# Kernel tuning notes

Measured on AMD Instinct MI355X. Metric: run time of the kernel, lower is better.

## Reference

```python
import jax, jax.numpy as jnp
import numpy as np
import math

B, NPG, DEG = 100, 500, 12          # graphs, nodes/graph, avg degree
F_IN, H, C = 128, 128, 10
RATIO = 0.5
N = B * NPG
E = N * DEG
K1 = math.ceil(NPG * RATIO)          # 250
K2 = math.ceil(K1 * RATIO)           # 125
K3 = math.ceil(K2 * RATIO)           # 63


def _lin(k, i, o):
    return jax.random.uniform(k, (i, o), jnp.float32, -1.0, 1.0) / np.sqrt(i).astype(np.float32)


def setup_inputs() -> dict:
    key = jax.random.key(0)
    ks = jax.random.split(key, 16)
    x = jax.random.normal(ks[0], (N, F_IN), jnp.float32)
    off = (jnp.arange(B, dtype=jnp.int32) * NPG)[:, None]
    src = (jax.random.randint(ks[1], (B, NPG * DEG), 0, NPG, jnp.int32) + off).reshape(-1)
    dst = (jax.random.randint(ks[2], (B, NPG * DEG), 0, NPG, jnp.int32) + off).reshape(-1)
    edge_index = jnp.stack([src, dst])
    return {
        'x': x, 'edge_index': edge_index,
        'Wl1': _lin(ks[3], F_IN, H), 'bl1': jnp.zeros((H,), jnp.float32), 'Wr1': _lin(ks[4], F_IN, H),
        'Wl2': _lin(ks[5], H, H), 'bl2': jnp.zeros((H,), jnp.float32), 'Wr2': _lin(ks[6], H, H),
        'Wl3': _lin(ks[7], H, H), 'bl3': jnp.zeros((H,), jnp.float32), 'Wr3': _lin(ks[8], H, H),
        'pw1': jax.random.normal(ks[9], (H,), jnp.float32),
        'pw2': jax.random.normal(ks[10], (H,), jnp.float32),
        'pw3': jax.random.normal(ks[11], (H,), jnp.float32),
        'W1': _lin(ks[12], 2 * H, H), 'b1': jnp.zeros((H,), jnp.float32),
        'W2': _lin(ks[13], H, H // 2), 'b2': jnp.zeros((H // 2,), jnp.float32),
        'W3': _lin(ks[14], H // 2, C), 'b3': jnp.zeros((C,), jnp.float32),
    }


def sage_conv(x, src, dst, emask, Wl, bl, Wr, n_nodes):
    # PyG SAGEConv: out_i = lin_l(mean_{j->i} x_j) + lin_r(x_i)
    msg = x[src] * emask[:, None]                                   # [E, d]
    agg = jax.ops.segment_sum(msg, dst, num_segments=n_nodes)
    cnt = jax.ops.segment_sum(emask, dst, num_segments=n_nodes)
    mean = agg / jnp.maximum(cnt, 1.0)[:, None]
    return mean @ Wl + bl + x @ Wr


def topk_pool(x, w, src, dst, emask, n_per, k):
    # TopKPooling: score = tanh(x.w/||w||); keep top-k nodes per graph; x_kept *= score
    score = jnp.tanh((x @ w) / jnp.linalg.norm(w))                  # [B*n_per]
    topv, topi = jax.lax.top_k(score.reshape(B, n_per), k)          # [B, k]
    perm = (topi + (jnp.arange(B, dtype=jnp.int32) * n_per)[:, None]).reshape(-1)
    x_new = x[perm] * topv.reshape(-1)[:, None]                     # [B*k, d]
    mapping = jnp.full((B * n_per,), -1, jnp.int32).at[perm].set(jnp.arange(B * k, dtype=jnp.int32))
    ns, nd = mapping[src], mapping[dst]
    emask_new = emask * ((ns >= 0) & (nd >= 0)).astype(emask.dtype)
    return x_new, jnp.maximum(ns, 0), jnp.maximum(nd, 0), emask_new


def readout(x, k):
    # global_max_pool || global_mean_pool (all graphs have exactly k nodes)
    xr = x.reshape(B, k, H)
    return jnp.concatenate([xr.max(axis=1), xr.mean(axis=1)], axis=1)  # [B, 2H]


def reference(x, edge_index, Wl1, bl1, Wr1, Wl2, bl2, Wr2, Wl3, bl3, Wr3,
              pw1, pw2, pw3, W1, b1, W2, b2, W3, b3):
    src, dst = edge_index[0], edge_index[1]
    emask = jnp.ones((E,), jnp.float32)
    h = jax.nn.relu(sage_conv(x, src, dst, emask, Wl1, bl1, Wr1, N))
    h, src, dst, emask = topk_pool(h, pw1, src, dst, emask, NPG, K1)
    x1 = readout(h, K1)
    h = jax.nn.relu(sage_conv(h, src, dst, emask, Wl2, bl2, Wr2, B * K1))
    h, src, dst, emask = topk_pool(h, pw2, src, dst, emask, K1, K2)
    x2 = readout(h, K2)
    h = jax.nn.relu(sage_conv(h, src, dst, emask, Wl3, bl3, Wr3, B * K2))
    h, src, dst, emask = topk_pool(h, pw3, src, dst, emask, K2, K3)
    x3 = readout(h, K3)
    z = x1 + x2 + x3
    z = jax.nn.relu(z @ W1 + b1)   # dropout is identity in eval mode
    z = jax.nn.relu(z @ W2 + b2)
    return jax.nn.log_softmax(z @ W3 + b3, axis=1)   # pool_loss == 0 for TopKPool
```

## Files before the change

### kernel.cpp

```cpp
#include <hip/hip_runtime.h>
#include <math.h>

#define BG    100
#define NPG   500
#define FD    128
#define EE    600000
#define EPG   6000
#define NN    50000
#define K1    250
#define K2    125
#define K3    63
#define CAP   64

typedef short v8s __attribute__((ext_vector_type(8)));
typedef float v4f __attribute__((ext_vector_type(4)));

__device__ __forceinline__ int swz(int p, int N) {
    int j = p & 7, i = p >> 3;
    int chunk = N >> 3, rem = N & 7;
    int mj = j < rem ? j : rem;
    return j * chunk + mj + i;
}

__device__ __forceinline__ unsigned short f2bf(float f) {
    unsigned int u = __float_as_uint(f);
    unsigned int r = (u + 0x7FFFu + ((u >> 16) & 1u)) >> 16;
    return (unsigned short)r;
}
__device__ __forceinline__ float bf2f(unsigned short b) {
    return __uint_as_float(((unsigned int)b) << 16);
}

__global__ void prep_w_kernel(const float* __restrict__ Wl1, const float* __restrict__ Wr1,
                              const float* __restrict__ Wl2, const float* __restrict__ Wr2,
                              const float* __restrict__ Wl3, const float* __restrict__ Wr3,
                              unsigned short* __restrict__ wt_hi, unsigned short* __restrict__ wt_lo) {
    int id = blockIdx.x * blockDim.x + threadIdx.x;
    if (id >= 3 * 256 * 128) return;
    int layer = id >> 15, rem = id & 32767;
    int k = rem >> 7, n = rem & 127;
    const float* Wl = layer == 0 ? Wl1 : (layer == 1 ? Wl2 : Wl3);
    const float* Wr = layer == 0 ? Wr1 : (layer == 1 ? Wr2 : Wr3);
    float w = (k < 128) ? Wl[k * 128 + n] : Wr[(k - 128) * 128 + n];
    unsigned short hi = f2bf(w);
    unsigned short lo = f2bf(w - bf2f(hi));
    long long o = (long long)layer * 32768 + n * 256 + k;
    wt_hi[o] = hi;
    wt_lo[o] = lo;
}

__global__ __launch_bounds__(1024) void fill_first_kernel(const int* __restrict__ ei,
                                                          int* __restrict__ deg,
                                                          int* __restrict__ col) {
    __shared__ int lcnt[NPG];
    int b = swz(blockIdx.x, BG), tid = threadIdx.x;
    for (int i = tid; i < NPG; i += 1024) lcnt[i] = 0;
    __syncthreads();
    for (int e0 = tid; e0 < EPG; e0 += 1024) {
        int e = b * EPG + e0;
        int d = ei[EE + e];
        int pos = atomicAdd(&lcnt[d - b * NPG], 1);
        if (pos < CAP) col[(long long)d * CAP + pos] = ei[e];
    }
    __syncthreads();
    for (int i = tid; i < NPG; i += 1024) deg[b * NPG + i] = lcnt[i];
}

__global__ void gather_agg_kernel(const int* __restrict__ deg, const int* __restrict__ col,
                                  const float* __restrict__ x, float* __restrict__ mean,
                                  int n, int NB) {
    int g = swz(blockIdx.x, NB) * 256 + threadIdx.x;
    int node = g >> 5, sub = g & 31;
    if (node >= n) return;
    int d = deg[node]; if (d > CAP) d = CAP;
    const int* cp = col + (long long)node * CAP;
    float ax = 0.0f, ay = 0.0f, az = 0.0f, aw = 0.0f;
    int j = 0;
    for (; j + 4 <= d; j += 4) {
        int s0 = cp[j], s1 = cp[j + 1], s2 = cp[j + 2], s3 = cp[j + 3];
        float4 v0 = ((const float4*)(x + (long long)s0 * FD))[sub];
        float4 v1 = ((const float4*)(x + (long long)s1 * FD))[sub];
        float4 v2 = ((const float4*)(x + (long long)s2 * FD))[sub];
        float4 v3 = ((const float4*)(x + (long long)s3 * FD))[sub];
        ax += v0.x; ay += v0.y; az += v0.z; aw += v0.w;
        ax += v1.x; ay += v1.y; az += v1.z; aw += v1.w;
        ax += v2.x; ay += v2.y; az += v2.z; aw += v2.w;
        ax += v3.x; ay += v3.y; az += v3.z; aw += v3.w;
    }
    for (; j < d; ++j) {
        float4 v = ((const float4*)(x + (long long)cp[j] * FD))[sub];
        ax += v.x; ay += v.y; az += v.z; aw += v.w;
    }
    float inv = 1.0f / fmaxf((float)d, 1.0f);
    float4 o; o.x = ax * inv; o.y = ay * inv; o.z = az * inv; o.w = aw * inv;
    ((float4*)(mean + (long long)node * FD))[sub] = o;
}

__global__ __launch_bounds__(256) void sage_gemm_mfma_kernel(
        const float* __restrict__ mean, const float* __restrict__ x,
        const unsigned short* __restrict__ wt_hi, const unsigned short* __restrict__ wt_lo,
        const float* __restrict__ bl, const float* __restrict__ pw,
        float* __restrict__ hout, float* __restrict__ score, int M, int NB) {
    __shared__ unsigned short Ah[64 * 40], Al[64 * 40];
    __shared__ unsigned short Bh[128 * 40], Bl[128 * 40];
    __shared__ float spart[64 * 16];
    __shared__ float snrmp[16];
    int tid  = threadIdx.x;
    int wave = tid >> 6, lane = tid & 63;
    int quad = lane >> 4, l15 = lane & 15;
    int row0 = swz(blockIdx.x, NB) * 64;

    v4f acc[8];
#pragma unroll
    for (int t = 0; t < 8; t++) acc[t] = (v4f){0.f, 0.f, 0.f, 0.f};

    if (tid < 16) {
        float s = 0.f;
#pragma unroll
        for (int t = 0; t < 8; t++) { float p = pw[t * 16 + tid]; s += p * p; }
        snrmp[tid] = s;
    }

    int arow = tid >> 2;
    int ak   = (tid & 3) * 8;
    int growA = row0 + arow; if (growA > M - 1) growA = M - 1;
    int brow = tid >> 1;
    int bk   = (tid & 1) * 16;

    for (int kt = 0; kt < 8; ++kt) {
        {
            const float* Ab = (kt < 4) ? mean : x;
            const float* ap = Ab + (long long)growA * FD + ((kt < 4) ? kt : kt - 4) * 32 + ak;
            float4 v0 = *(const float4*)(ap);
            float4 v1 = *(const float4*)(ap + 4);
            float f[8] = {v0.x, v0.y, v0.z, v0.w, v1.x, v1.y, v1.z, v1.w};
            ushort4 h0, h1, l0, l1;
            unsigned short hb[8], lb[8];
#pragma unroll
            for (int q = 0; q < 8; q++) {
                hb[q] = f2bf(f[q]);
                lb[q] = f2bf(f[q] - bf2f(hb[q]));
            }
            h0 = make_ushort4(hb[0], hb[1], hb[2], hb[3]);
            h1 = make_ushort4(hb[4], hb[5], hb[6], hb[7]);
            l0 = make_ushort4(lb[0], lb[1], lb[2], lb[3]);
            l1 = make_ushort4(lb[4], lb[5], lb[6], lb[7]);
            *(ushort4*)&Ah[arow * 40 + ak]     = h0;
            *(ushort4*)&Ah[arow * 40 + ak + 4] = h1;
            *(ushort4*)&Al[arow * 40 + ak]     = l0;
            *(ushort4*)&Al[arow * 40 + ak + 4] = l1;
        }
        {
            int klog = kt * 32;
            const uint4* sh = (const uint4*)(wt_hi + (long long)brow * 256 + klog + bk);
            const uint4* sl = (const uint4*)(wt_lo + (long long)brow * 256 + klog + bk);
            uint4 vh0 = sh[0], vh1 = sh[1];
            uint4 vl0 = sl[0], vl1 = sl[1];
            *(uint4*)&Bh[brow * 40 + bk]     = vh0;
            *(uint4*)&Bh[brow * 40 + bk + 8] = vh1;
            *(uint4*)&Bl[brow * 40 + bk]     = vl0;
            *(uint4*)&Bl[brow * 40 + bk + 8] = vl1;
        }
        __syncthreads();
        v8s a_h = *(const v8s*)&Ah[(16 * wave + l15) * 40 + quad * 8];
        v8s a_l = *(const v8s*)&Al[(16 * wave + l15) * 40 + quad * 8];
#pragma unroll
        for (int t = 0; t < 8; t++) {
            v8s b_h = *(const v8s*)&Bh[(t * 16 + l15) * 40 + quad * 8];
            v8s b_l = *(const v8s*)&Bl[(t * 16 + l15) * 40 + quad * 8];
            acc[t] = __builtin_amdgcn_mfma_f32_16x16x32_bf16(a_l, b_h, acc[t], 0, 0, 0);
            acc[t] = __builtin_amdgcn_mfma_f32_16x16x32_bf16(a_h, b_l, acc[t], 0, 0, 0);
            acc[t] = __builtin_amdgcn_mfma_f32_16x16x32_bf16(a_h, b_h, acc[t], 0, 0, 0);
        }
        __syncthreads();
    }

    int rbase = row0 + 16 * wave + quad * 4;
    float part[4] = {0.f, 0.f, 0.f, 0.f};
#pragma unroll
    for (int t = 0; t < 8; t++) {
        int colc = t * 16 + l15;
        float blv = bl[colc];
        float pwv = pw[colc];
#pragma unroll
        for (int reg = 0; reg < 4; reg++) {
            float h = fmaxf(acc[t][reg] + blv, 0.0f);
            part[reg] += h * pwv;
            int grow = rbase + reg;
            if (grow < M) hout[(long long)grow * FD + colc] = h;
        }
    }
#pragma unroll
    for (int reg = 0; reg < 4; reg++)
        spart[(16 * wave + quad * 4 + reg) * 16 + l15] = part[reg];
    __syncthreads();
    if (tid < 64) {
        int grow = row0 + tid;
        if (grow < M) {
            float dot = 0.0f;
#pragma unroll
            for (int i = 0; i < 16; i++) dot += spart[tid * 16 + i];
            float nr = 0.0f;
#pragma unroll
            for (int i = 0; i < 16; i++) nr += snrmp[i];
            score[grow] = tanhf(dot / sqrtf(nr));
        }
    }
}

__global__ __launch_bounds__(1024) void topk_tail_kernel(
        const float* __restrict__ score, const float* __restrict__ hout,
        int n_per, int k, int SN,
        float* __restrict__ xp,
        const int* __restrict__ esrc, const int* __restrict__ edst,
        const float* __restrict__ em_in,
        int* __restrict__ src_out, int* __restrict__ dst_out, float* __restrict__ em_out,
        int* __restrict__ next_deg, int* __restrict__ next_col,
        float* __restrict__ z, int mode,
        const float* __restrict__ W1, const float* __restrict__ b1,
        const float* __restrict__ W2, const float* __restrict__ b2,
        const float* __restrict__ W3, const float* __restrict__ b3,
        float* __restrict__ out) {
    __shared__ float skey[512];
    __shared__ int   sidx[512];
    __shared__ int   lmap[512];
    __shared__ int   lcnt[512];
    __shared__ float pmax[1024];
    __shared__ float psum[1024];
    __shared__ float zs[256], t1[128], t2[64], t3[16];
    int b = swz(blockIdx.x, BG), tid = threadIdx.x;

    for (int i = tid; i < SN; i += 1024) {
        if (i < n_per) { skey[i] = score[b * n_per + i]; sidx[i] = i; }
        else           { skey[i] = -INFINITY;            sidx[i] = 0x7fffffff; }
        lmap[i] = -1;
        lcnt[i] = 0;
    }
    __syncthreads();

    for (int ks = 2; ks <= SN; ks <<= 1) {
        for (int j = ks >> 1; j > 0; j >>= 1) {
            for (int i = tid; i < SN; i += 1024) {
                int l = i ^ j;
                if (l > i) {
                    float ki = skey[i], kl = skey[l];
                    int   ii = sidx[i], il = sidx[l];
                    bool before = (ki > kl) || (ki == kl && ii < il);
                    bool up = ((i & ks) == 0);
                    if (up ? !before : before) {
                        skey[i] = kl; skey[l] = ki;
                        sidx[i] = il; sidx[l] = ii;
                    }
                }
            }
            __syncthreads();
        }
    }

    for (int i = tid; i < k; i += 1024) lmap[sidx[i]] = i;
    __syncthreads();

    if (esrc) {
        int nbase = b * n_per, kbase = b * k;
        for (int e0 = tid; e0 < EPG; e0 += 1024) {
            int e = b * EPG + e0;
            bool alive = em_in ? (em_in[e] != 0.0f) : true;
            if (alive) {
                int ls = lmap[esrc[e] - nbase];
                int ld = lmap[edst[e] - nbase];
                bool keep = (ls >= 0) && (ld >= 0);
                if (keep) {
                    int pos = atomicAdd(&lcnt[ld], 1);
                    if (pos < CAP) next_col[(long long)(kbase + ld) * CAP + pos] = kbase + ls;
                }
                if (em_out) {
                    em_out[e]  = keep ? 1.0f : 0.0f;
                    src_out[e] = keep ? kbase + ls : 0;
                    dst_out[e] = keep ? kbase + ld : 0;
                }
            } else if (em_out) {
                em_out[e] = 0.0f; src_out[e] = 0; dst_out[e] = 0;
            }
        }
        __syncthreads();
        for (int i = tid; i < k; i += 1024) next_deg[b * k + i] = lcnt[i];
    }

    int c = tid & 127, s = tid >> 7;
    float mx = -INFINITY, sm = 0.0f;
    {
        int r = s;
        long long hbase = (long long)b * n_per * FD + c;
        long long xbase = (long long)b * k * FD + c;
        for (; r + 24 < k; r += 32) {
            int i0 = sidx[r], i1 = sidx[r + 8], i2 = sidx[r + 16], i3 = sidx[r + 24];
            float k0 = skey[r], k1 = skey[r + 8], k2 = skey[r + 16], k3 = skey[r + 24];
            float v0 = hout[hbase + (long long)i0 * FD] * k0;
            float v1 = hout[hbase + (long long)i1 * FD] * k1;
            float v2 = hout[hbase + (long long)i2 * FD] * k2;
            float v3 = hout[hbase + (long long)i3 * FD] * k3;
            xp[xbase + (long long)(r)      * FD] = v0;
            xp[xbase + (long long)(r + 8)  * FD] = v1;
            xp[xbase + (long long)(r + 16) * FD] = v2;
            xp[xbase + (long long)(r + 24) * FD] = v3;
            mx = fmaxf(mx, v0); sm += v0;
            mx = fmaxf(mx, v1); sm += v1;
            mx = fmaxf(mx, v2); sm += v2;
            mx = fmaxf(mx, v3); sm += v3;
        }
        for (; r < k; r += 8) {
            float v = hout[hbase + (long long)sidx[r] * FD] * skey[r];
            xp[xbase + (long long)r * FD] = v;
            mx = fmaxf(mx, v); sm += v;
        }
    }
    pmax[tid] = mx; psum[tid] = sm;
    __syncthreads();
    if (tid < 128) {
        float m = -INFINITY, su = 0.0f;
#pragma unroll
        for (int i = 0; i < 8; i++) {
            m = fmaxf(m, pmax[i * 128 + tid]);
            su += psum[i * 128 + tid];
        }
        float mean = su / (float)k;
        if (mode == 0)      { z[b * 256 + tid] = m;  z[b * 256 + 128 + tid] = mean;  }
        else if (mode == 1) { z[b * 256 + tid] += m; z[b * 256 + 128 + tid] += mean; }
        else {
            zs[tid]       = z[b * 256 + tid] + m;
            zs[128 + tid] = z[b * 256 + 128 + tid] + mean;
        }
    }
    if (mode == 2) {
        __syncthreads();
        if (tid < 128) {
            float a = b1[tid];
            for (int kk = 0; kk < 256; kk++) a += zs[kk] * W1[kk * 128 + tid];
            t1[tid] = fmaxf(a, 0.0f);
        }
        __syncthreads();
        if (tid < 64) {
            float a = b2[tid];
            for (int kk = 0; kk < 128; kk++) a += t1[kk] * W2[kk * 64 + tid];
            t2[tid] = fmaxf(a, 0.0f);
        }
        __syncthreads();
        if (tid < 10) {
            float a = b3[tid];
            for (int kk = 0; kk < 64; kk++) a += t2[kk] * W3[kk * 10 + tid];
            t3[tid] = a;
        }
        __syncthreads();
        if (tid == 0) {
            float m = -INFINITY;
            for (int i = 0; i < 10; i++) m = fmaxf(m, t3[i]);
            float su = 0.0f;
            for (int i = 0; i < 10; i++) su += expf(t3[i] - m);
            float ls = logf(su);
            for (int i = 0; i < 10; i++) out[b * 10 + i] = t3[i] - m - ls;
        }
    }
}

extern "C" void kernel_launch(void* const* d_in, const int* in_sizes, int n_in,
                              void* d_out, int out_size, void* d_ws, size_t ws_size,
                              hipStream_t stream) {
    (void)in_sizes; (void)n_in; (void)out_size; (void)ws_size;
    const float* x   = (const float*)d_in[0];
    const int*   ei  = (const int*)d_in[1];
    const float* Wl1 = (const float*)d_in[2];
    const float* bl1 = (const float*)d_in[3];
    const float* Wr1 = (const float*)d_in[4];
    const float* Wl2 = (const float*)d_in[5];
    const float* bl2 = (const float*)d_in[6];
    const float* Wr2 = (const float*)d_in[7];
    const float* Wl3 = (const float*)d_in[8];
    const float* bl3 = (const float*)d_in[9];
    const float* Wr3 = (const float*)d_in[10];
    const float* pw1 = (const float*)d_in[11];
    const float* pw2 = (const float*)d_in[12];
    const float* pw3 = (const float*)d_in[13];
    const float* W1  = (const float*)d_in[14];
    const float* b1  = (const float*)d_in[15];
    const float* W2  = (const float*)d_in[16];
    const float* b2  = (const float*)d_in[17];
    const float* W3  = (const float*)d_in[18];
    const float* b3  = (const float*)d_in[19];
    float* out = (float*)d_out;

    char* ws = (char*)d_ws;
    size_t off = 0;
    auto alloc = [&](size_t bytes) {
        char* p = ws + off;
        off = (off + bytes + 255) & ~(size_t)255;
        return p;
    };
    float* mean  = (float*)alloc((size_t)NN * FD * 4);
    float* hout  = (float*)alloc((size_t)NN * FD * 4);
    float* xp    = (float*)alloc((size_t)BG * K1 * FD * 4);
    float* sc    = (float*)alloc((size_t)NN * 4);
    int*   srcb  = (int*)  alloc((size_t)EE * 4);
    int*   dstb  = (int*)  alloc((size_t)EE * 4);
    float* emb   = (float*)alloc((size_t)EE * 4);
    int*   deg   = (int*)  alloc((size_t)NN * 4);
    int*   colb  = (int*)  alloc((size_t)NN * CAP * 4);
    float* z     = (float*)alloc((size_t)BG * 256 * 4);
    unsigned short* wt_hi = (unsigned short*)alloc((size_t)3 * 32768 * 2);
    unsigned short* wt_lo = (unsigned short*)alloc((size_t)3 * 32768 * 2);

    prep_w_kernel<<<(3 * 32768 + 255) / 256, 256, 0, stream>>>(Wl1, Wr1, Wl2, Wr2, Wl3, Wr3,
                                                               wt_hi, wt_lo);
    fill_first_kernel<<<BG, 1024, 0, stream>>>(ei, deg, colb);

    {
        int nb = (NN * 32 + 255) / 256;
        gather_agg_kernel<<<nb, 256, 0, stream>>>(deg, colb, x, mean, NN, nb);
    }
    {
        int nb = (NN + 63) / 64;
        sage_gemm_mfma_kernel<<<nb, 256, 0, stream>>>(mean, x, wt_hi, wt_lo,
                                                      bl1, pw1, hout, sc, NN, nb);
    }
    topk_tail_kernel<<<BG, 1024, 0, stream>>>(sc, hout, NPG, K1, 512, xp,
                                              ei, ei + EE, (const float*)0,
                                              srcb, dstb, emb, deg, colb,
                                              z, 0, W1, b1, W2, b2, W3, b3, out);

    const int N2 = BG * K1;
    {
        int nb = (N2 * 32 + 255) / 256;
        gather_agg_kernel<<<nb, 256, 0, stream>>>(deg, colb, xp, mean, N2, nb);
    }
    {
        int nb = (N2 + 63) / 64;
        sage_gemm_mfma_kernel<<<nb, 256, 0, stream>>>(mean, xp, wt_hi + 32768, wt_lo + 32768,
                                                      bl2, pw2, hout, sc, N2, nb);
    }
    topk_tail_kernel<<<BG, 1024, 0, stream>>>(sc, hout, K1, K2, 256, xp,
                                              srcb, dstb, emb,
                                              (int*)0, (int*)0, (float*)0, deg, colb,
                                              z, 1, W1, b1, W2, b2, W3, b3, out);

    const int N3 = BG * K2;
    {
        int nb = (N3 * 32 + 255) / 256;
        gather_agg_kernel<<<nb, 256, 0, stream>>>(deg, colb, xp, mean, N3, nb);
    }
    {
        int nb = (N3 + 63) / 64;
        sage_gemm_mfma_kernel<<<nb, 256, 0, stream>>>(mean, xp, wt_hi + 65536, wt_lo + 65536,
                                                      bl3, pw3, hout, sc, N3, nb);
    }
    topk_tail_kernel<<<BG, 1024, 0, stream>>>(sc, hout, K2, K3, 128, xp,
                                              (const int*)0, (const int*)0, (const float*)0,
                                              (int*)0, (int*)0, (float*)0, (int*)0, (int*)0,
                                              z, 2, W1, b1, W2, b2, W3, b3, out);
}
```

Measured before the change: 269.9 us.

## Merge weight prep into edge-fill kernel and load GEMM A fragments directly

Two changes. First, the weight split/transpose kernel and the first-layer adjacency fill kernel are merged into one launch, with the extra blocks doing weight prep, which removes one kernel launch. Second, the SAGE GEMM no longer stages the A operand through shared memory: each lane loads its own fp32 A fragment straight from global memory and splits it into bf16 hi/lo in registers, dropping the A LDS buffers and their writes and reads. The cost is that global A loads are less coalesced, since each lane reads 32 contiguous bytes from its own row.

```diff
diff --git a/kernel.cpp b/kernel.cpp
--- a/kernel.cpp
+++ b/kernel.cpp
@@ -31,39 +31,40 @@
     return __uint_as_float(((unsigned int)b) << 16);
 }
 
-__global__ void prep_w_kernel(const float* __restrict__ Wl1, const float* __restrict__ Wr1,
-                              const float* __restrict__ Wl2, const float* __restrict__ Wr2,
-                              const float* __restrict__ Wl3, const float* __restrict__ Wr3,
-                              unsigned short* __restrict__ wt_hi, unsigned short* __restrict__ wt_lo) {
-    int id = blockIdx.x * blockDim.x + threadIdx.x;
-    if (id >= 3 * 256 * 128) return;
-    int layer = id >> 15, rem = id & 32767;
-    int k = rem >> 7, n = rem & 127;
-    const float* Wl = layer == 0 ? Wl1 : (layer == 1 ? Wl2 : Wl3);
-    const float* Wr = layer == 0 ? Wr1 : (layer == 1 ? Wr2 : Wr3);
-    float w = (k < 128) ? Wl[k * 128 + n] : Wr[(k - 128) * 128 + n];
-    unsigned short hi = f2bf(w);
-    unsigned short lo = f2bf(w - bf2f(hi));
-    long long o = (long long)layer * 32768 + n * 256 + k;
-    wt_hi[o] = hi;
-    wt_lo[o] = lo;
-}
-
-__global__ __launch_bounds__(1024) void fill_first_kernel(const int* __restrict__ ei,
-                                                          int* __restrict__ deg,
-                                                          int* __restrict__ col) {
+__global__ __launch_bounds__(1024) void prep_fill_kernel(
+        const int* __restrict__ ei, int* __restrict__ deg, int* __restrict__ col,
+        const float* __restrict__ Wl1, const float* __restrict__ Wr1,
+        const float* __restrict__ Wl2, const float* __restrict__ Wr2,
+        const float* __restrict__ Wl3, const float* __restrict__ Wr3,
+        unsigned short* __restrict__ wt_hi, unsigned short* __restrict__ wt_lo) {
     __shared__ int lcnt[NPG];
-    int b = swz(blockIdx.x, BG), tid = threadIdx.x;
-    for (int i = tid; i < NPG; i += 1024) lcnt[i] = 0;
-    __syncthreads();
-    for (int e0 = tid; e0 < EPG; e0 += 1024) {
-        int e = b * EPG + e0;
-        int d = ei[EE + e];
-        int pos = atomicAdd(&lcnt[d - b * NPG], 1);
-        if (pos < CAP) col[(long long)d * CAP + pos] = ei[e];
-    }
-    __syncthreads();
-    for (int i = tid; i < NPG; i += 1024) deg[b * NPG + i] = lcnt[i];
+    int tid = threadIdx.x;
+    if (blockIdx.x < BG) {
+        int b = swz(blockIdx.x, BG);
+        for (int i = tid; i < NPG; i += 1024) lcnt[i] = 0;
+        __syncthreads();
+        for (int e0 = tid; e0 < EPG; e0 += 1024) {
+            int e = b * EPG + e0;
+            int d = ei[EE + e];
+            int pos = atomicAdd(&lcnt[d - b * NPG], 1);
+            if (pos < CAP) col[(long long)d * CAP + pos] = ei[e];
+        }
+        __syncthreads();
+        for (int i = tid; i < NPG; i += 1024) deg[b * NPG + i] = lcnt[i];
+    } else {
+        int id = (blockIdx.x - BG) * 1024 + tid;
+        if (id >= 3 * 256 * 128) return;
+        int layer = id >> 15, rem = id & 32767;
+        int k = rem >> 7, n = rem & 127;
+        const float* Wl = layer == 0 ? Wl1 : (layer == 1 ? Wl2 : Wl3);
+        const float* Wr = layer == 0 ? Wr1 : (layer == 1 ? Wr2 : Wr3);
+        float w = (k < 128) ? Wl[k * 128 + n] : Wr[(k - 128) * 128 + n];
+        unsigned short hi = f2bf(w);
+        unsigned short lo = f2bf(w - bf2f(hi));
+        long long o = (long long)layer * 32768 + n * 256 + k;
+        wt_hi[o] = hi;
+        wt_lo[o] = lo;
+    }
 }
 
 __global__ void gather_agg_kernel(const int* __restrict__ deg, const int* __restrict__ col,
@@ -101,7 +102,6 @@
         const unsigned short* __restrict__ wt_hi, const unsigned short* __restrict__ wt_lo,
         const float* __restrict__ bl, const float* __restrict__ pw,
         float* __restrict__ hout, float* __restrict__ score, int M, int NB) {
-    __shared__ unsigned short Ah[64 * 40], Al[64 * 40];
     __shared__ unsigned short Bh[128 * 40], Bl[128 * 40];
     __shared__ float spart[64 * 16];
     __shared__ float snrmp[16];
@@ -121,35 +121,15 @@
         snrmp[tid] = s;
     }
 
-    int arow = tid >> 2;
-    int ak   = (tid & 3) * 8;
-    int growA = row0 + arow; if (growA > M - 1) growA = M - 1;
+    int growA = row0 + 16 * wave + l15; if (growA > M - 1) growA = M - 1;
     int brow = tid >> 1;
     int bk   = (tid & 1) * 16;
 
     for (int kt = 0; kt < 8; ++kt) {
-        {
-            const float* Ab = (kt < 4) ? mean : x;
-            const float* ap = Ab + (long long)growA * FD + ((kt < 4) ? kt : kt - 4) * 32 + ak;
-            float4 v0 = *(const float4*)(ap);
-            float4 v1 = *(const float4*)(ap + 4);
-            float f[8] = {v0.x, v0.y, v0.z, v0.w, v1.x, v1.y, v1.z, v1.w};
-            ushort4 h0, h1, l0, l1;
-            unsigned short hb[8], lb[8];
-#pragma unroll
-            for (int q = 0; q < 8; q++) {
-                hb[q] = f2bf(f[q]);
-                lb[q] = f2bf(f[q] - bf2f(hb[q]));
-            }
-            h0 = make_ushort4(hb[0], hb[1], hb[2], hb[3]);
-            h1 = make_ushort4(hb[4], hb[5], hb[6], hb[7]);
-            l0 = make_ushort4(lb[0], lb[1], lb[2], lb[3]);
-            l1 = make_ushort4(lb[4], lb[5], lb[6], lb[7]);
-            *(ushort4*)&Ah[arow * 40 + ak]     = h0;
-            *(ushort4*)&Ah[arow * 40 + ak + 4] = h1;
-            *(ushort4*)&Al[arow * 40 + ak]     = l0;
-            *(ushort4*)&Al[arow * 40 + ak + 4] = l1;
-        }
+        const float* Ab = (kt < 4) ? mean : x;
+        const float* ap = Ab + (long long)growA * FD + ((kt < 4) ? kt : kt - 4) * 32 + quad * 8;
+        float4 v0 = *(const float4*)(ap);
+        float4 v1 = *(const float4*)(ap + 4);
         {
             int klog = kt * 32;
             const uint4* sh = (const uint4*)(wt_hi + (long long)brow * 256 + klog + bk);
@@ -161,9 +141,15 @@
             *(uint4*)&Bl[brow * 40 + bk]     = vl0;
             *(uint4*)&Bl[brow * 40 + bk + 8] = vl1;
         }
-        __syncthreads();
-        v8s a_h = *(const v8s*)&Ah[(16 * wave + l15) * 40 + quad * 8];
-        v8s a_l = *(const v8s*)&Al[(16 * wave + l15) * 40 + quad * 8];
+        float f[8] = {v0.x, v0.y, v0.z, v0.w, v1.x, v1.y, v1.z, v1.w};
+        v8s a_h, a_l;
+#pragma unroll
+        for (int q = 0; q < 8; q++) {
+            unsigned short hb = f2bf(f[q]);
+            a_h[q] = (short)hb;
+            a_l[q] = (short)f2bf(f[q] - bf2f(hb));
+        }
+        __syncthreads();
 #pragma unroll
         for (int t = 0; t < 8; t++) {
             v8s b_h = *(const v8s*)&Bh[(t * 16 + l15) * 40 + quad * 8];
@@ -408,9 +394,8 @@
     unsigned short* wt_hi = (unsigned short*)alloc((size_t)3 * 32768 * 2);
     unsigned short* wt_lo = (unsigned short*)alloc((size_t)3 * 32768 * 2);
 
-    prep_w_kernel<<<(3 * 32768 + 255) / 256, 256, 0, stream>>>(Wl1, Wr1, Wl2, Wr2, Wl3, Wr3,
-                                                               wt_hi, wt_lo);
-    fill_first_kernel<<<BG, 1024, 0, stream>>>(ei, deg, colb);
+    prep_fill_kernel<<<BG + 96, 1024, 0, stream>>>(ei, deg, colb,
+                                                   Wl1, Wr1, Wl2, Wr2, Wl3, Wr3, wt_hi, wt_lo);
 
     {
         int nb = (NN * 32 + 255) / 256;
```

Measured after the change: 267.1 us. No clear change (-1.0%).
